# Kernel tuning notes

Hardware: AMD Instinct MI355X
Metric: run time of the kernel (lower is better)

Reference implementation:

```python
import jax, jax.numpy as jnp
import numpy as np

N_NODES = 20000
N_EDGES = 640000
D_IN = 128
D_OUT = 128


def setup_inputs() -> dict:
    key = jax.random.key(0)
    k1, k2, k3, k4 = jax.random.split(key, 4)
    x = jax.random.normal(k1, (N_NODES, D_IN), dtype=jnp.float32)
    edge_index = jax.random.randint(k2, (2, N_EDGES), 0, N_NODES, dtype=jnp.int64)
    edge_weight = jnp.ones((N_EDGES,), dtype=jnp.float32)
    # Linear(in_feats, out_feats) params (PyTorch convention: W [out, in])
    bound = 1.0 / np.sqrt(D_IN)
    W = jax.random.uniform(k3, (D_OUT, D_IN), minval=-bound, maxval=bound, dtype=jnp.float32)
    b = jax.random.uniform(k4, (D_OUT,), minval=-bound, maxval=bound, dtype=jnp.float32)
    return {"x": x, "edge_index": edge_index, "edge_weight": edge_weight, "W": W, "b": b}


def reference(x, edge_index, edge_weight, W, b):
    # MeanAggregator: h = Linear(x); out = row-normalized spmm(adj, h)
    h = x @ W.T + b  # [N, D_OUT]
    row, col = edge_index[0], edge_index[1]
    # message = w_ij * h[j], scattered into row i  (spmm with COO adjacency)
    msg = h[col] * edge_weight[:, None]  # [E, D_OUT]
    agg = jax.ops.segment_sum(msg, row, num_segments=N_NODES)  # [N, D_OUT]
    deg = jax.ops.segment_sum(edge_weight, row, num_segments=N_NODES)  # [N]
    deg_inv = jnp.where(deg > 0, 1.0 / deg, 0.0)
    out = agg * deg_inv[:, None]
    # normalize=True -> F.normalize(out, p=2, dim=-1)
    norm = jnp.linalg.norm(out, axis=-1, keepdims=True)
    out = out / jnp.maximum(norm, 1e-12)
    return out
```

## Files before the change

kernel.cpp:

```cpp
#include <hip/hip_runtime.h>
#include <hip/hip_bf16.h>
#include <math.h>

#define N_NODES 20000
#define N_EDGES 640000
#define D 128

#define BSHIFT 5
#define BNODES 32
#define NBUCK 625
#define CAP 1536
#define AGG_T 512
#define SRPT 3
#define NBLK1 320
#define CHUNK 2000
#define GPAD 16

#define GROWS 16

typedef __attribute__((ext_vector_type(8))) short bf16x8;
typedef __attribute__((ext_vector_type(4))) float f32x4;

static __device__ __forceinline__ unsigned short f2bf(float f) {
  unsigned u = __float_as_uint(f);
  return (unsigned short)((u + 0x7fffu + ((u >> 16) & 1u)) >> 16);
}
static __device__ __forceinline__ float bflo(unsigned v) {
  return __uint_as_float(v << 16);
}
static __device__ __forceinline__ float bfhi(unsigned v) {
  return __uint_as_float(v & 0xffff0000u);
}

__global__ __launch_bounds__(256) void cast_kernel(
    const float* __restrict__ x, const float* __restrict__ W,
    unsigned* __restrict__ xb, unsigned* __restrict__ Wb,
    int* __restrict__ gcur) {
  const int i = blockIdx.x * 256 + threadIdx.x;
  if (i < N_NODES * D / 4) {
    const float4 v = *reinterpret_cast<const float4*>(&x[(size_t)i * 4]);
    uint2 o;
    o.x = (unsigned)f2bf(v.x) | ((unsigned)f2bf(v.y) << 16);
    o.y = (unsigned)f2bf(v.z) | ((unsigned)f2bf(v.w) << 16);
    *reinterpret_cast<uint2*>(&xb[(size_t)i * 2]) = o;
  }
  if (i < D * D / 4) {
    const float4 v = *reinterpret_cast<const float4*>(&W[(size_t)i * 4]);
    uint2 o;
    o.x = (unsigned)f2bf(v.x) | ((unsigned)f2bf(v.y) << 16);
    o.y = (unsigned)f2bf(v.z) | ((unsigned)f2bf(v.w) << 16);
    *reinterpret_cast<uint2*>(&Wb[(size_t)i * 2]) = o;
  }
  if (i < NBUCK * GPAD) gcur[i] = 0;
}

__global__ __launch_bounds__(256) void bin_kernel(
    const int* __restrict__ rows, const int* __restrict__ cols,
    const float* __restrict__ ew, int* __restrict__ gcur,
    uint2* __restrict__ bins) {
  __shared__ int cnt[NBUCK];
  __shared__ int basep[NBUCK];
  const int tid = threadIdx.x;
  const int e0 = blockIdx.x * CHUNK;
  for (int i = tid; i < NBUCK; i += 256) cnt[i] = 0;
  __syncthreads();
  const int4* r4 = reinterpret_cast<const int4*>(rows + e0);
  for (int t = tid; t < CHUNK / 4; t += 256) {
    const int4 rv = r4[t];
    atomicAdd(&cnt[rv.x >> BSHIFT], 1);
    atomicAdd(&cnt[rv.y >> BSHIFT], 1);
    atomicAdd(&cnt[rv.z >> BSHIFT], 1);
    atomicAdd(&cnt[rv.w >> BSHIFT], 1);
  }
  __syncthreads();
  for (int i = tid; i < NBUCK; i += 256) {
    const int c = cnt[i];
    basep[i] = c ? atomicAdd(&gcur[i * GPAD], c) : 0;
  }
  __syncthreads();
  for (int i = tid; i < NBUCK; i += 256) cnt[i] = 0;
  __syncthreads();
  for (int t = tid; t < CHUNK / 4; t += 256) {
    const int4 rv = r4[t];
    const int4 cv = reinterpret_cast<const int4*>(cols + e0)[t];
    const float4 wv = reinterpret_cast<const float4*>(ew + e0)[t];
    const int rr[4] = {rv.x, rv.y, rv.z, rv.w};
    const int cc[4] = {cv.x, cv.y, cv.z, cv.w};
    const float ww[4] = {wv.x, wv.y, wv.z, wv.w};
#pragma unroll
    for (int u = 0; u < 4; ++u) {
      const int b = rr[u] >> BSHIFT;
      const int p = basep[b] + atomicAdd(&cnt[b], 1);
      if (p < CAP)
        bins[(size_t)b * CAP + p] =
            make_uint2(((unsigned)(rr[u] & (BNODES - 1)) << 16) | (unsigned)cc[u],
                       __float_as_uint(ww[u]));
    }
  }
}

__global__ __launch_bounds__(AGG_T) void agg_gemm_kernel(
    const unsigned* __restrict__ xb, const int* __restrict__ gcur,
    const uint2* __restrict__ bins, const unsigned* __restrict__ Wb,
    const float* __restrict__ bias, float* __restrict__ out) {
  __shared__ uint2 list[CAP];
  __shared__ unsigned aggls[BNODES * 64];
  __shared__ int cnt[BNODES];
  __shared__ int base[BNODES];
  __shared__ float degls[BNODES];
  const int b = blockIdx.x;
  const int tid = threadIdx.x;
  const int n = min(gcur[b * GPAD], CAP);
  if (tid < BNODES) cnt[tid] = 0;
  __syncthreads();

  uint2 ebuf[SRPT];
  int rkbuf[SRPT], rlbuf[SRPT];
#pragma unroll
  for (int j = 0; j < SRPT; ++j) {
    const int i = tid + j * AGG_T;
    rlbuf[j] = -1;
    if (i < n) {
      const uint2 e = bins[(size_t)b * CAP + i];
      const int rl = (int)(e.x >> 16);
      ebuf[j] = e;
      rlbuf[j] = rl;
      rkbuf[j] = atomicAdd(&cnt[rl], 1);
    }
  }
  __syncthreads();
  if (tid < 64) {
    const int c = (tid < BNODES) ? cnt[tid] : 0;
    int s = c;
#pragma unroll
    for (int off = 1; off < BNODES; off <<= 1) {
      const int t = __shfl_up(s, off);
      if (tid >= off) s += t;
    }
    if (tid < BNODES) base[tid] = s - c;
  }
  __syncthreads();
#pragma unroll
  for (int j = 0; j < SRPT; ++j)
    if (rlbuf[j] >= 0) {
      const int p = base[rlbuf[j]] + rkbuf[j];
      if (p < CAP) list[p] = ebuf[j];
    }
  __syncthreads();

  const int wv = tid >> 6, lane = tid & 63;
  const int q4 = lane >> 4, fidx = lane & 15;
  for (int q = 0; q < 4; ++q) {
    const int rl = wv * 4 + q;
    const int s = base[rl];
    const int ke = min(s + cnt[rl], CAP);
    float a[8] = {0.f, 0.f, 0.f, 0.f, 0.f, 0.f, 0.f, 0.f};
    float dw = 0.f;
    for (int k = s; k < ke; k += 32) {
      uint4 v[8];
      float w[8];
#pragma unroll
      for (int u = 0; u < 8; ++u) {
        int idx = k + u * 4 + q4;
        const bool ok = idx < ke;
        if (!ok) idx = ke - 1;
        const uint2 e = list[idx];
        w[u] = ok ? __uint_as_float(e.y) : 0.f;
        v[u] = *reinterpret_cast<const uint4*>(
            &xb[(size_t)(e.x & 0xffffu) * (D / 2) + fidx * 4]);
      }
#pragma unroll
      for (int u = 0; u < 8; ++u) {
        a[0] += bflo(v[u].x) * w[u]; a[1] += bfhi(v[u].x) * w[u];
        a[2] += bflo(v[u].y) * w[u]; a[3] += bfhi(v[u].y) * w[u];
        a[4] += bflo(v[u].z) * w[u]; a[5] += bfhi(v[u].z) * w[u];
        a[6] += bflo(v[u].w) * w[u]; a[7] += bfhi(v[u].w) * w[u];
        dw += w[u];
      }
    }
#pragma unroll
    for (int j = 0; j < 8; ++j) {
      a[j] += __shfl_xor(a[j], 16);
      a[j] += __shfl_xor(a[j], 32);
    }
    dw += __shfl_xor(dw, 16);
    dw += __shfl_xor(dw, 32);
    const float dinv = dw > 0.f ? 1.f / dw : 0.f;
    if (lane == 0) degls[rl] = dw;
    if (q4 == 0) {
      uint4 o;
      o.x = (unsigned)f2bf(a[0] * dinv) | ((unsigned)f2bf(a[1] * dinv) << 16);
      o.y = (unsigned)f2bf(a[2] * dinv) | ((unsigned)f2bf(a[3] * dinv) << 16);
      o.z = (unsigned)f2bf(a[4] * dinv) | ((unsigned)f2bf(a[5] * dinv) << 16);
      o.w = (unsigned)f2bf(a[6] * dinv) | ((unsigned)f2bf(a[7] * dinv) << 16);
      *reinterpret_cast<uint4*>(
          &aggls[rl * 64 + ((fidx * 4) ^ ((rl & 7) << 2))]) = o;
    }
  }
  __syncthreads();

  if (wv >= 2) return;
  const int arow = wv * 16 + (lane & 15);
  const int koff = (lane >> 4) * 4;

  bf16x8 afr[4];
#pragma unroll
  for (int kk = 0; kk < 4; ++kk) {
    const int wbase = (kk * 16 + koff) ^ ((arow & 7) << 2);
    union { uint4 u; bf16x8 v; } cv;
    cv.u = *reinterpret_cast<const uint4*>(&aggls[arow * 64 + wbase]);
    afr[kk] = cv.v;
  }

  f32x4 acc[8];
#pragma unroll
  for (int t = 0; t < 8; ++t) {
    const int o = t * 16 + (lane & 15);
    f32x4 c = {0.f, 0.f, 0.f, 0.f};
#pragma unroll
    for (int kk = 0; kk < 4; ++kk) {
      union { uint4 u; bf16x8 v; } cv;
      cv.u = *reinterpret_cast<const uint4*>(
          &Wb[(size_t)o * (D / 2) + kk * 16 + koff]);
      c = __builtin_amdgcn_mfma_f32_16x16x32_bf16(afr[kk], cv.v, c, 0, 0, 0);
    }
    acc[t] = c;
  }

  float ss[4] = {0.f, 0.f, 0.f, 0.f};
#pragma unroll
  for (int t = 0; t < 8; ++t) {
    const float bc = bias[t * 16 + (lane & 15)];
#pragma unroll
    for (int r = 0; r < 4; ++r) {
      const float y = acc[t][r] + bc;
      acc[t][r] = y;
      ss[r] += y * y;
    }
  }
#pragma unroll
  for (int r = 0; r < 4; ++r) {
#pragma unroll
    for (int off = 1; off < 16; off <<= 1)
      ss[r] += __shfl_xor(ss[r], off);
  }
  float scale[4];
#pragma unroll
  for (int r = 0; r < 4; ++r) {
    const int lrow = wv * 16 + (lane >> 4) * 4 + r;
    const float dw = degls[lrow];
    scale[r] = (dw > 0.f) ? 1.f / fmaxf(sqrtf(ss[r]), 1e-12f) : 0.f;
  }
#pragma unroll
  for (int t = 0; t < 8; ++t) {
#pragma unroll
    for (int r = 0; r < 4; ++r) {
      const int lrow = wv * 16 + (lane >> 4) * 4 + r;
      out[(size_t)(b * BNODES + lrow) * D + t * 16 + (lane & 15)] =
          acc[t][r] * scale[r];
    }
  }
}

__global__ __launch_bounds__(256) void scatter_kernel(
    const float* __restrict__ x, const int* __restrict__ rows,
    const int* __restrict__ cols, const float* __restrict__ ew,
    float* __restrict__ out, float* __restrict__ degw) {
  const int e = blockIdx.x * 4 + (threadIdx.x >> 6);
  const int lane = threadIdx.x & 63;
  if (e >= N_EDGES) return;
  const int r = rows[e];
  const int c = cols[e];
  const float w = ew[e];
  const float2 v = *reinterpret_cast<const float2*>(&x[(size_t)c * D + lane * 2]);
  atomicAdd(&out[(size_t)r * D + lane * 2], v.x * w);
  atomicAdd(&out[(size_t)r * D + lane * 2 + 1], v.y * w);
  if (lane == 0) atomicAdd(&degw[r], w);
}

__global__ __launch_bounds__(256) void linear_norm_kernel(
    const float* __restrict__ W, const float* __restrict__ b,
    const float* __restrict__ degw, float* __restrict__ out) {
  __shared__ float Ws[D][D + 1];
  __shared__ float xs[GROWS][D];
  __shared__ float dws[GROWS];
  const int tid = threadIdx.x;
  const int row0 = blockIdx.x * GROWS;
  for (int idx = tid; idx < D * D; idx += 256)
    Ws[idx >> 7][idx & 127] = W[idx];
  if (tid < GROWS) dws[tid] = degw[row0 + tid];
  __syncthreads();
  for (int idx = tid; idx < GROWS * D; idx += 256) {
    const int r = idx >> 7;
    const float dw = dws[r];
    const float dinv = dw > 0.f ? 1.f / dw : 0.f;
    xs[r][idx & 127] = out[(size_t)(row0 + r) * D + (idx & 127)] * dinv;
  }
  __syncthreads();
  const int o = tid & 127;
  const int rh = tid >> 7;
  float acc[GROWS / 2];
#pragma unroll
  for (int j = 0; j < GROWS / 2; ++j) acc[j] = 0.f;
  for (int k = 0; k < D; ++k) {
    const float wv = Ws[o][k];
#pragma unroll
    for (int j = 0; j < GROWS / 2; ++j)
      acc[j] += xs[rh + 2 * j][k] * wv;
  }
  const float bias = b[o];
  __syncthreads();
#pragma unroll
  for (int j = 0; j < GROWS / 2; ++j)
    xs[rh + 2 * j][o] = acc[j] + bias;
  __syncthreads();
  const int w = tid >> 6, lane = tid & 63;
#pragma unroll
  for (int q = 0; q < 4; ++q) {
    const int r = w * 4 + q;
    const float2 v = *reinterpret_cast<const float2*>(&xs[r][lane * 2]);
    float ss = v.x * v.x + v.y * v.y;
#pragma unroll
    for (int off = 1; off < 64; off <<= 1) ss += __shfl_xor(ss, off);
    const float dw = dws[r];
    const float scale = (dw > 0.f) ? 1.f / fmaxf(sqrtf(ss), 1e-12f) : 0.f;
    *reinterpret_cast<float2*>(&out[(size_t)(row0 + r) * D + lane * 2]) =
        make_float2(v.x * scale, v.y * scale);
  }
}

extern "C" void kernel_launch(void* const* d_in, const int* in_sizes, int n_in,
                              void* d_out, int out_size, void* d_ws, size_t ws_size,
                              hipStream_t stream) {
  const float* x  = (const float*)d_in[0];
  const int*   ei = (const int*)d_in[1];
  const float* ew = (const float*)d_in[2];
  const float* W  = (const float*)d_in[3];
  const float* b  = (const float*)d_in[4];
  float* out = (float*)d_out;
  char* ws = (char*)d_ws;

  const int* rows = ei;
  const int* cols = ei + N_EDGES;

  size_t off = 0;
  int* gcur = (int*)(ws + off);        off += (size_t)NBUCK * GPAD * 4;
  float* degw = (float*)(ws + off);    off += (size_t)N_NODES * 4;
  unsigned* xb = (unsigned*)(ws + off);  off += (size_t)N_NODES * (D / 2) * 4;
  unsigned* Wb = (unsigned*)(ws + off);  off += (size_t)D * (D / 2) * 4;
  uint2* bins = (uint2*)(ws + off);    off += (size_t)NBUCK * CAP * 8;
  const size_t main_bytes = off;
  const size_t fallback_bytes = (size_t)NBUCK * GPAD * 4 + (size_t)N_NODES * 4;

  if (ws_size >= main_bytes) {
    cast_kernel<<<(N_NODES * D / 4 + 255) / 256, 256, 0, stream>>>(x, W, xb, Wb, gcur);
    bin_kernel<<<NBLK1, 256, 0, stream>>>(rows, cols, ew, gcur, bins);
    agg_gemm_kernel<<<NBUCK, AGG_T, 0, stream>>>(xb, gcur, bins, Wb, b, out);
  } else if (ws_size >= fallback_bytes) {
    hipMemsetAsync(out, 0, (size_t)N_NODES * D * 4, stream);
    hipMemsetAsync(degw, 0, (size_t)N_NODES * 4, stream);
    scatter_kernel<<<(N_EDGES + 3) / 4, 256, 0, stream>>>(x, rows, cols, ew, out, degw);
    linear_norm_kernel<<<N_NODES / GROWS, 256, 0, stream>>>(W, b, degw, out);
  }
}
```

Baseline: 67.77 us.

## Fuse cast and binning kernels and split aggregation blocks into node halves

The bf16 cast of x/W now runs in the same launch as the edge binning, handled by extra blocks, and the counter zeroing moves into a tiny separate kernel. The aggregation+GEMM kernel now launches two blocks per 32-node bucket, and each block keeps only the edges of its 16-node half. This doubles the grid and halves shared memory per block to raise occupancy. In exchange every block reads the full bucket of edges and discards half of them. Only one wave per block does the MFMA stage, and each wave aggregates 2 rows instead of 4.

Result: faster. 63.30 us (-6.6%).

```diff
diff --git a/kernel.cpp b/kernel.cpp
--- a/kernel.cpp
+++ b/kernel.cpp
@@ -10,11 +10,14 @@
 #define BNODES 32
 #define NBUCK 625
 #define CAP 1536
+#define HNOD 16
+#define HCAP 768
 #define AGG_T 512
 #define SRPT 3
 #define NBLK1 320
 #define CHUNK 2000
 #define GPAD 16
+#define CASTBLK 2500
 
 #define GROWS 16
 
@@ -32,69 +35,72 @@
   return __uint_as_float(v & 0xffff0000u);
 }
 
-__global__ __launch_bounds__(256) void cast_kernel(
+__global__ __launch_bounds__(256) void zero_kernel(int* __restrict__ p, int n) {
+  const int i = blockIdx.x * 256 + threadIdx.x;
+  if (i < n) p[i] = 0;
+}
+
+__global__ __launch_bounds__(256) void castbin_kernel(
     const float* __restrict__ x, const float* __restrict__ W,
+    const int* __restrict__ rows, const int* __restrict__ cols,
+    const float* __restrict__ ew,
     unsigned* __restrict__ xb, unsigned* __restrict__ Wb,
-    int* __restrict__ gcur) {
-  const int i = blockIdx.x * 256 + threadIdx.x;
-  if (i < N_NODES * D / 4) {
-    const float4 v = *reinterpret_cast<const float4*>(&x[(size_t)i * 4]);
-    uint2 o;
-    o.x = (unsigned)f2bf(v.x) | ((unsigned)f2bf(v.y) << 16);
-    o.y = (unsigned)f2bf(v.z) | ((unsigned)f2bf(v.w) << 16);
-    *reinterpret_cast<uint2*>(&xb[(size_t)i * 2]) = o;
-  }
-  if (i < D * D / 4) {
-    const float4 v = *reinterpret_cast<const float4*>(&W[(size_t)i * 4]);
-    uint2 o;
-    o.x = (unsigned)f2bf(v.x) | ((unsigned)f2bf(v.y) << 16);
-    o.y = (unsigned)f2bf(v.z) | ((unsigned)f2bf(v.w) << 16);
-    *reinterpret_cast<uint2*>(&Wb[(size_t)i * 2]) = o;
-  }
-  if (i < NBUCK * GPAD) gcur[i] = 0;
-}
-
-__global__ __launch_bounds__(256) void bin_kernel(
-    const int* __restrict__ rows, const int* __restrict__ cols,
-    const float* __restrict__ ew, int* __restrict__ gcur,
-    uint2* __restrict__ bins) {
+    int* __restrict__ gcur, uint2* __restrict__ bins) {
   __shared__ int cnt[NBUCK];
   __shared__ int basep[NBUCK];
   const int tid = threadIdx.x;
-  const int e0 = blockIdx.x * CHUNK;
-  for (int i = tid; i < NBUCK; i += 256) cnt[i] = 0;
-  __syncthreads();
-  const int4* r4 = reinterpret_cast<const int4*>(rows + e0);
-  for (int t = tid; t < CHUNK / 4; t += 256) {
-    const int4 rv = r4[t];
-    atomicAdd(&cnt[rv.x >> BSHIFT], 1);
-    atomicAdd(&cnt[rv.y >> BSHIFT], 1);
-    atomicAdd(&cnt[rv.z >> BSHIFT], 1);
-    atomicAdd(&cnt[rv.w >> BSHIFT], 1);
-  }
-  __syncthreads();
-  for (int i = tid; i < NBUCK; i += 256) {
-    const int c = cnt[i];
-    basep[i] = c ? atomicAdd(&gcur[i * GPAD], c) : 0;
-  }
-  __syncthreads();
-  for (int i = tid; i < NBUCK; i += 256) cnt[i] = 0;
-  __syncthreads();
-  for (int t = tid; t < CHUNK / 4; t += 256) {
-    const int4 rv = r4[t];
-    const int4 cv = reinterpret_cast<const int4*>(cols + e0)[t];
-    const float4 wv = reinterpret_cast<const float4*>(ew + e0)[t];
-    const int rr[4] = {rv.x, rv.y, rv.z, rv.w};
-    const int cc[4] = {cv.x, cv.y, cv.z, cv.w};
-    const float ww[4] = {wv.x, wv.y, wv.z, wv.w};
-#pragma unroll
-    for (int u = 0; u < 4; ++u) {
-      const int b = rr[u] >> BSHIFT;
-      const int p = basep[b] + atomicAdd(&cnt[b], 1);
-      if (p < CAP)
-        bins[(size_t)b * CAP + p] =
-            make_uint2(((unsigned)(rr[u] & (BNODES - 1)) << 16) | (unsigned)cc[u],
-                       __float_as_uint(ww[u]));
+  if (blockIdx.x < NBLK1) {
+    const int e0 = blockIdx.x * CHUNK;
+    for (int i = tid; i < NBUCK; i += 256) cnt[i] = 0;
+    __syncthreads();
+    const int4* r4 = reinterpret_cast<const int4*>(rows + e0);
+    for (int t = tid; t < CHUNK / 4; t += 256) {
+      const int4 rv = r4[t];
+      atomicAdd(&cnt[rv.x >> BSHIFT], 1);
+      atomicAdd(&cnt[rv.y >> BSHIFT], 1);
+      atomicAdd(&cnt[rv.z >> BSHIFT], 1);
+      atomicAdd(&cnt[rv.w >> BSHIFT], 1);
+    }
+    __syncthreads();
+    for (int i = tid; i < NBUCK; i += 256) {
+      const int c = cnt[i];
+      basep[i] = c ? atomicAdd(&gcur[i * GPAD], c) : 0;
+    }
+    __syncthreads();
+    for (int i = tid; i < NBUCK; i += 256) cnt[i] = 0;
+    __syncthreads();
+    for (int t = tid; t < CHUNK / 4; t += 256) {
+      const int4 rv = r4[t];
+      const int4 cv = reinterpret_cast<const int4*>(cols + e0)[t];
+      const float4 wv = reinterpret_cast<const float4*>(ew + e0)[t];
+      const int rr[4] = {rv.x, rv.y, rv.z, rv.w};
+      const int cc[4] = {cv.x, cv.y, cv.z, cv.w};
+      const float ww[4] = {wv.x, wv.y, wv.z, wv.w};
+#pragma unroll
+      for (int u = 0; u < 4; ++u) {
+        const int b = rr[u] >> BSHIFT;
+        const int p = basep[b] + atomicAdd(&cnt[b], 1);
+        if (p < CAP)
+          bins[(size_t)b * CAP + p] =
+              make_uint2(((unsigned)(rr[u] & (BNODES - 1)) << 16) | (unsigned)cc[u],
+                         __float_as_uint(ww[u]));
+      }
+    }
+  } else {
+    const int i = (blockIdx.x - NBLK1) * 256 + tid;
+    if (i < N_NODES * D / 4) {
+      const float4 v = *reinterpret_cast<const float4*>(&x[(size_t)i * 4]);
+      uint2 o;
+      o.x = (unsigned)f2bf(v.x) | ((unsigned)f2bf(v.y) << 16);
+      o.y = (unsigned)f2bf(v.z) | ((unsigned)f2bf(v.w) << 16);
+      *reinterpret_cast<uint2*>(&xb[(size_t)i * 2]) = o;
+    }
+    if (i < D * D / 4) {
+      const float4 v = *reinterpret_cast<const float4*>(&W[(size_t)i * 4]);
+      uint2 o;
+      o.x = (unsigned)f2bf(v.x) | ((unsigned)f2bf(v.y) << 16);
+      o.y = (unsigned)f2bf(v.z) | ((unsigned)f2bf(v.w) << 16);
+      *reinterpret_cast<uint2*>(&Wb[(size_t)i * 2]) = o;
     }
   }
 }
@@ -103,15 +109,16 @@
     const unsigned* __restrict__ xb, const int* __restrict__ gcur,
     const uint2* __restrict__ bins, const unsigned* __restrict__ Wb,
     const float* __restrict__ bias, float* __restrict__ out) {
-  __shared__ uint2 list[CAP];
-  __shared__ unsigned aggls[BNODES * 64];
-  __shared__ int cnt[BNODES];
-  __shared__ int base[BNODES];
-  __shared__ float degls[BNODES];
-  const int b = blockIdx.x;
+  __shared__ uint2 list[HCAP];
+  __shared__ unsigned aggls[HNOD * 64];
+  __shared__ int cnt[HNOD];
+  __shared__ int base[HNOD];
+  __shared__ float degls[HNOD];
+  const int b = blockIdx.x >> 1;
+  const int half = blockIdx.x & 1;
   const int tid = threadIdx.x;
   const int n = min(gcur[b * GPAD], CAP);
-  if (tid < BNODES) cnt[tid] = 0;
+  if (tid < HNOD) cnt[tid] = 0;
   __syncthreads();
 
   uint2 ebuf[SRPT];
@@ -123,37 +130,39 @@
     if (i < n) {
       const uint2 e = bins[(size_t)b * CAP + i];
       const int rl = (int)(e.x >> 16);
-      ebuf[j] = e;
-      rlbuf[j] = rl;
-      rkbuf[j] = atomicAdd(&cnt[rl], 1);
+      if ((rl >> 4) == half) {
+        ebuf[j] = e;
+        rlbuf[j] = rl & 15;
+        rkbuf[j] = atomicAdd(&cnt[rl & 15], 1);
+      }
     }
   }
   __syncthreads();
   if (tid < 64) {
-    const int c = (tid < BNODES) ? cnt[tid] : 0;
+    const int c = (tid < HNOD) ? cnt[tid] : 0;
     int s = c;
 #pragma unroll
-    for (int off = 1; off < BNODES; off <<= 1) {
+    for (int off = 1; off < HNOD; off <<= 1) {
       const int t = __shfl_up(s, off);
       if (tid >= off) s += t;
     }
-    if (tid < BNODES) base[tid] = s - c;
+    if (tid < HNOD) base[tid] = s - c;
   }
   __syncthreads();
 #pragma unroll
   for (int j = 0; j < SRPT; ++j)
     if (rlbuf[j] >= 0) {
       const int p = base[rlbuf[j]] + rkbuf[j];
-      if (p < CAP) list[p] = ebuf[j];
+      if (p < HCAP) list[p] = ebuf[j];
     }
   __syncthreads();
 
   const int wv = tid >> 6, lane = tid & 63;
   const int q4 = lane >> 4, fidx = lane & 15;
-  for (int q = 0; q < 4; ++q) {
-    const int rl = wv * 4 + q;
+  for (int q = 0; q < 2; ++q) {
+    const int rl = wv * 2 + q;
     const int s = base[rl];
-    const int ke = min(s + cnt[rl], CAP);
+    const int ke = min(s + cnt[rl], HCAP);
     float a[8] = {0.f, 0.f, 0.f, 0.f, 0.f, 0.f, 0.f, 0.f};
     float dw = 0.f;
     for (int k = s; k < ke; k += 32) {
@@ -199,8 +208,8 @@
   }
   __syncthreads();
 
-  if (wv >= 2) return;
-  const int arow = wv * 16 + (lane & 15);
+  if (wv != 0) return;
+  const int arow = lane & 15;
   const int koff = (lane >> 4) * 4;
 
   bf16x8 afr[4];
@@ -244,10 +253,11 @@
     for (int off = 1; off < 16; off <<= 1)
       ss[r] += __shfl_xor(ss[r], off);
   }
+  const int row0 = b * BNODES + half * HNOD;
   float scale[4];
 #pragma unroll
   for (int r = 0; r < 4; ++r) {
-    const int lrow = wv * 16 + (lane >> 4) * 4 + r;
+    const int lrow = (lane >> 4) * 4 + r;
     const float dw = degls[lrow];
     scale[r] = (dw > 0.f) ? 1.f / fmaxf(sqrtf(ss[r]), 1e-12f) : 0.f;
   }
@@ -255,8 +265,8 @@
   for (int t = 0; t < 8; ++t) {
 #pragma unroll
     for (int r = 0; r < 4; ++r) {
-      const int lrow = wv * 16 + (lane >> 4) * 4 + r;
-      out[(size_t)(b * BNODES + lrow) * D + t * 16 + (lane & 15)] =
+      const int lrow = (lane >> 4) * 4 + r;
+      out[(size_t)(row0 + lrow) * D + t * 16 + (lane & 15)] =
           acc[t][r] * scale[r];
     }
   }
@@ -353,9 +363,10 @@
   const size_t fallback_bytes = (size_t)NBUCK * GPAD * 4 + (size_t)N_NODES * 4;
 
   if (ws_size >= main_bytes) {
-    cast_kernel<<<(N_NODES * D / 4 + 255) / 256, 256, 0, stream>>>(x, W, xb, Wb, gcur);
-    bin_kernel<<<NBLK1, 256, 0, stream>>>(rows, cols, ew, gcur, bins);
-    agg_gemm_kernel<<<NBUCK, AGG_T, 0, stream>>>(xb, gcur, bins, Wb, b, out);
+    zero_kernel<<<(NBUCK * GPAD + 255) / 256, 256, 0, stream>>>(gcur, NBUCK * GPAD);
+    castbin_kernel<<<NBLK1 + CASTBLK, 256, 0, stream>>>(x, W, rows, cols, ew,
+                                                        xb, Wb, gcur, bins);
+    agg_gemm_kernel<<<NBUCK * 2, AGG_T, 0, stream>>>(xb, gcur, bins, Wb, b, out);
   } else if (ws_size >= fallback_bytes) {
     hipMemsetAsync(out, 0, (size_t)N_NODES * D * 4, stream);
     hipMemsetAsync(degw, 0, (size_t)N_NODES * 4, stream);
```
